# Kernel tuning notes

Hardware: AMD Instinct MI355X
Metric: run time of the kernel (lower is better)

Reference implementation:

```python
import jax, jax.numpy as jnp
import numpy as np

N = 500_000   # total nodes in batched graph
E = 10_000_000  # total edges
G = 1_000     # number of graphs in the batch
H = 8         # hidden_dim
C = 8         # n_classes


def setup_inputs() -> dict:
    key = jax.random.key(0)
    k1, k2, k3, k4, k5, k6 = jax.random.split(key, 6)
    src = jax.random.randint(k1, (E,), 0, N)
    dst = jax.random.randint(k2, (E,), 0, N)
    graph_ids = jnp.sort(jax.random.randint(k3, (N,), 0, G))
    W1 = jax.random.normal(k4, (1, H), dtype=jnp.float32) * 0.5
    W2 = jax.random.normal(k5, (H, H), dtype=jnp.float32) * 0.3
    Wlast = jax.random.normal(k6, (H, C), dtype=jnp.float32) * 0.3
    return {"W1": W1, "W2": W2, "Wlast": Wlast,
            "src": src, "dst": dst, "graph_ids": graph_ids}


def reference(W1, W2, Wlast, src, dst, graph_ids):
    ones_e = jnp.ones(src.shape[0], dtype=jnp.float32)
    deg_in = jax.ops.segment_sum(ones_e, dst, num_segments=N)   # in-degrees
    deg_out = jax.ops.segment_sum(ones_e, src, num_segments=N)  # out-degrees
    # DGL GraphConv norm='both': clamp degrees to >=1, then pow(-1/2)
    inv_sqrt_out = jnp.maximum(deg_out, 1.0) ** -0.5
    inv_sqrt_in = jnp.maximum(deg_in, 1.0) ** -0.5

    def gconv(h, W):
        # h: [N, d]; gather-scatter message passing, then dense transform
        h = h * inv_sqrt_out[:, None]
        agg = jax.ops.segment_sum(h[src], dst, num_segments=N)
        return (agg * inv_sqrt_in[:, None]) @ W

    h = deg_in[:, None]  # input feature = in_degrees, shape [N, 1]
    h = jax.nn.relu(gconv(h, W1))
    h = jax.nn.relu(gconv(h, W2))

    # dgl.mean_nodes: per-graph mean over nodes
    counts = jax.ops.segment_sum(jnp.ones(N, dtype=jnp.float32), graph_ids,
                                 num_segments=G)
    hg = jax.ops.segment_sum(h, graph_ids, num_segments=G)
    hg = hg / jnp.maximum(counts, 1.0)[:, None]
    return hg @ Wlast  # [G, n_classes], Linear with bias=False
```

## Files before the change

kernel.cpp:

```cpp
#include <hip/hip_runtime.h>


#define TB 256
#define DTB 512
#define STB 512
#define BSH 13
#define BNODES 8192
#define MAXNB 64
#define SCH 4096
#define SCH4 (SCH / 4)
#define SCH2 4096
#define EPT 8
#define CSTR 16
#define GLG 4
#define GNUM 16
#define INVB 0xFFFFFFFFu

typedef __attribute__((ext_vector_type(4))) int int4v;
typedef __attribute__((ext_vector_type(4))) unsigned uint4v;
typedef __attribute__((ext_vector_type(2))) unsigned uint2v;
typedef __attribute__((ext_vector_type(4))) float float4v;

__global__ void init_kernel(unsigned* __restrict__ curD, unsigned* __restrict__ curS,
                            unsigned* __restrict__ curC, float* __restrict__ Xsum,
                            int NB, unsigned CAP, int cells, unsigned CAP2, int G) {
    int i = blockIdx.x * TB + threadIdx.x;
    if (i < NB) curD[i * CSTR] = (unsigned)i * CAP;
    if (curS && i < NB) curS[i * CSTR] = (unsigned)i * CAP;
    if (curC && i < cells) curC[i * CSTR] = (unsigned)i * CAP2;
    if (i < G) Xsum[i] = 0.0f;
}

__global__ void scatter_sort_kernel(const int* __restrict__ src, const int* __restrict__ dst,
                                    unsigned* __restrict__ curD, unsigned* __restrict__ curS,
                                    unsigned* __restrict__ dstP, unsigned short* __restrict__ srcP,
                                    int NB, int E, int blk0) {
    __shared__ unsigned cntD[MAXNB], cntS[MAXNB];
    __shared__ unsigned deltaD[MAXNB], deltaS[MAXNB];
    __shared__ unsigned totD_s, totS_s;
    __shared__ unsigned payD[SCH];
    __shared__ unsigned short valS[SCH];
    __shared__ unsigned char mapD[SCH], mapS[SCH];

    int tid = threadIdx.x;
    if (tid < MAXNB) { cntD[tid] = 0u; cntS[tid] = 0u; }
    __syncthreads();

    unsigned sA[EPT], dA[EPT], bD[EPT], bS[EPT];
    int blk = blockIdx.x + blk0;
#pragma unroll
    for (int v = 0; v < 2; ++v) {
        int q = blk * SCH4 + v * STB + tid;
        int be = q * 4;
        if (be + 3 < E) {
            int4v s4 = __builtin_nontemporal_load((const int4v*)src + q);
            int4v d4 = __builtin_nontemporal_load((const int4v*)dst + q);
#pragma unroll
            for (int k = 0; k < 4; ++k) {
                sA[v*4+k] = (unsigned)s4[k];
                dA[v*4+k] = (unsigned)d4[k];
                bD[v*4+k] = dA[v*4+k] >> BSH;
                bS[v*4+k] = sA[v*4+k] >> BSH;
            }
        } else {
#pragma unroll
            for (int k = 0; k < 4; ++k) {
                int j = be + k;
                if (j < E) {
                    sA[v*4+k] = (unsigned)src[j];
                    dA[v*4+k] = (unsigned)dst[j];
                    bD[v*4+k] = dA[v*4+k] >> BSH;
                    bS[v*4+k] = sA[v*4+k] >> BSH;
                } else {
                    bD[v*4+k] = INVB; bS[v*4+k] = INVB;
                    sA[v*4+k] = 0u; dA[v*4+k] = 0u;
                }
            }
        }
    }

#pragma unroll
    for (int k = 0; k < EPT; ++k) {
        if (bD[k] != INVB) {
            atomicAdd(&cntD[bD[k]], 1u);
            if (srcP) atomicAdd(&cntS[bS[k]], 1u);
        }
    }
    __syncthreads();

    int wv = tid >> 6, ln = tid & 63;
    if (wv == 0) {
        unsigned x = (ln < NB) ? cntD[ln] : 0u;
        unsigned inc = x;
#pragma unroll
        for (int o = 1; o < 64; o <<= 1) {
            unsigned y = __shfl_up(inc, o, 64);
            if (ln >= o) inc += y;
        }
        unsigned exc = inc - x;
        if (ln < NB) {
            unsigned gb = atomicAdd(&curD[ln * CSTR], x);
            deltaD[ln] = gb - exc;
            cntD[ln] = exc;
        }
        if (ln == 63) totD_s = inc;
    } else if (wv == 1 && srcP) {
        unsigned x = (ln < NB) ? cntS[ln] : 0u;
        unsigned inc = x;
#pragma unroll
        for (int o = 1; o < 64; o <<= 1) {
            unsigned y = __shfl_up(inc, o, 64);
            if (ln >= o) inc += y;
        }
        unsigned exc = inc - x;
        if (ln < NB) {
            unsigned gb = atomicAdd(&curS[ln * CSTR], x);
            deltaS[ln] = gb - exc;
            cntS[ln] = exc;
        }
        if (ln == 63) totS_s = inc;
    }
    __syncthreads();

#pragma unroll
    for (int k = 0; k < EPT; ++k) {
        if (bD[k] != INVB) {
            unsigned p = atomicAdd(&cntD[bD[k]], 1u);
            payD[p] = ((dA[k] & (BNODES - 1)) << 19) | sA[k];
            mapD[p] = (unsigned char)bD[k];
            if (srcP) {
                unsigned p2 = atomicAdd(&cntS[bS[k]], 1u);
                valS[p2] = (unsigned short)(sA[k] & (BNODES - 1));
                mapS[p2] = (unsigned char)bS[k];
            }
        }
    }
    __syncthreads();

    unsigned tD = totD_s;
    for (unsigned i = tid; i < tD; i += STB) {
        unsigned b = mapD[i];
        dstP[deltaD[b] + i] = payD[i];
    }
    if (srcP) {
        unsigned tS = totS_s;
        for (unsigned i = tid; i < tS; i += STB) {
            unsigned b = mapS[i];
            srcP[deltaS[b] + i] = valS[i];
        }
    }
}

__global__ void subsort_kernel(const unsigned* __restrict__ dstP, const unsigned* __restrict__ curD,
                               unsigned* __restrict__ curC, unsigned* __restrict__ dstP2,
                               unsigned CAP, unsigned CAP2, int NB, int MAXCH) {
    __shared__ unsigned cnt2[MAXNB], delta2[MAXNB];
    __shared__ unsigned tot_s;
    __shared__ unsigned pay[SCH2];
    __shared__ unsigned char map2[SCH2];

    int db = blockIdx.x / MAXCH, c = blockIdx.x % MAXCH;
    unsigned s = (unsigned)db * CAP + (unsigned)c * SCH2;
    unsigned e = curD[db * CSTR];
    if (s >= e) return;
    unsigned n = e - s; if (n > SCH2) n = SCH2;

    int tid = threadIdx.x;
    if (tid < MAXNB) cnt2[tid] = 0u;
    __syncthreads();

    unsigned pl[EPT], bk[EPT];
#pragma unroll
    for (int v = 0; v < 2; ++v) {
        unsigned q = (unsigned)(v * STB + tid);
        unsigned base = q * 4u;
        if (base + 3u < n) {
            uint4v p4 = *((const uint4v*)(dstP + s) + q);
#pragma unroll
            for (int k = 0; k < 4; ++k) {
                pl[v*4+k] = p4[k];
                bk[v*4+k] = (p4[k] & 0x7FFFFu) >> BSH;
            }
        } else {
#pragma unroll
            for (int k = 0; k < 4; ++k) {
                unsigned j = base + (unsigned)k;
                if (j < n) {
                    pl[v*4+k] = dstP[s + j];
                    bk[v*4+k] = (pl[v*4+k] & 0x7FFFFu) >> BSH;
                } else { bk[v*4+k] = INVB; pl[v*4+k] = 0u; }
            }
        }
    }

#pragma unroll
    for (int k = 0; k < EPT; ++k)
        if (bk[k] != INVB) atomicAdd(&cnt2[bk[k]], 1u);
    __syncthreads();

    if (tid < 64) {
        int ln = tid;
        unsigned x = cnt2[ln];
        unsigned inc = x;
#pragma unroll
        for (int o = 1; o < 64; o <<= 1) {
            unsigned y = __shfl_up(inc, o, 64);
            if (ln >= o) inc += y;
        }
        unsigned exc = inc - x;
        if (ln < NB) {
            unsigned gb = atomicAdd(&curC[((unsigned)db * NB + ln) * CSTR], x);
            delta2[ln] = gb - exc;
            cnt2[ln] = exc;
        }
        if (ln == 63) tot_s = inc;
    }
    __syncthreads();

#pragma unroll
    for (int k = 0; k < EPT; ++k) {
        if (bk[k] != INVB) {
            unsigned p = atomicAdd(&cnt2[bk[k]], 1u);
            pay[p] = ((pl[k] >> 19) << BSH) | (pl[k] & (BNODES - 1));
            map2[p] = (unsigned char)bk[k];
        }
    }
    __syncthreads();

    unsigned tot = tot_s;
    for (unsigned i = tid; i < tot; i += STB) {
        unsigned b = map2[i];
        dstP2[delta2[b] + i] = pay[i];
    }
}

__global__ void deg2_kernel(const unsigned* __restrict__ dstP2, const unsigned* __restrict__ curC,
                            unsigned CAP2, unsigned* __restrict__ pDeg, int NB, int GS) {
    __shared__ unsigned h[BNODES];
    {
        uint4v* hv = (uint4v*)h;
        for (int t = threadIdx.x; t < BNODES / 4; t += DTB) hv[t] = (uint4v)0u;
    }
    __syncthreads();
    int b = blockIdx.x >> GLG, g = blockIdx.x & (GNUM - 1);
    int cEnd = (g + 1) * GS; if (cEnd > NB) cEnd = NB;
    for (int c = g * GS; c < cEnd; ++c) {
        unsigned cell = (unsigned)(b * NB + c);
        unsigned lo = cell * CAP2;
        unsigned hi = curC[cell * CSTR];
        unsigned i1 = hi & ~3u;
        const uint4v* qp = (const uint4v*)(dstP2 + lo);
        for (unsigned q = threadIdx.x; q < (i1 - lo) / 4u; q += DTB) {
            uint4v e4 = qp[q];
            atomicAdd(&h[e4.x >> BSH], 0x10000u);
            atomicAdd(&h[e4.y >> BSH], 0x10000u);
            atomicAdd(&h[e4.z >> BSH], 0x10000u);
            atomicAdd(&h[e4.w >> BSH], 0x10000u);
        }
        if (threadIdx.x < hi - i1)
            atomicAdd(&h[dstP2[i1 + threadIdx.x] >> BSH], 0x10000u);
    }
    for (int c = g * GS; c < cEnd; ++c) {
        unsigned cell = (unsigned)(c * NB + b);
        unsigned lo = cell * CAP2;
        unsigned hi = curC[cell * CSTR];
        unsigned i1 = hi & ~3u;
        const uint4v* qp = (const uint4v*)(dstP2 + lo);
        for (unsigned q = threadIdx.x; q < (i1 - lo) / 4u; q += DTB) {
            uint4v e4 = qp[q];
            atomicAdd(&h[e4.x & (BNODES - 1)], 1u);
            atomicAdd(&h[e4.y & (BNODES - 1)], 1u);
            atomicAdd(&h[e4.z & (BNODES - 1)], 1u);
            atomicAdd(&h[e4.w & (BNODES - 1)], 1u);
        }
        if (threadIdx.x < hi - i1)
            atomicAdd(&h[dstP2[i1 + threadIdx.x] & (BNODES - 1)], 1u);
    }
    __syncthreads();
    uint4v* rowv = (uint4v*)(pDeg + (size_t)blockIdx.x * BNODES);
    uint4v* hv = (uint4v*)h;
    for (int t = threadIdx.x; t < BNODES / 4; t += DTB) rowv[t] = hv[t];
}

__global__ void prep2_kernel(const unsigned* __restrict__ pDeg,
                             float* __restrict__ pio, float* __restrict__ h0s,
                             float* __restrict__ isiA, int Npad) {
    int i = blockIdx.x * TB + threadIdx.x;
    if (i >= Npad) return;
    int b = i >> BSH, l = i & (BNODES - 1);
    unsigned din_u = 0, dout_u = 0;
    for (int g = 0; g < GNUM; ++g) {
        unsigned v = __builtin_nontemporal_load(&pDeg[(size_t)(b * GNUM + g) * BNODES + l]);
        din_u  += v >> 16;
        dout_u += v & 0xFFFFu;
    }
    float din = (float)din_u, dout = (float)dout_u;
    float a  = 1.0f / sqrtf(fmaxf(din, 1.0f));
    float bo = 1.0f / sqrtf(fmaxf(dout, 1.0f));
    pio[i]  = a * bo;
    h0s[i]  = din * bo;
    isiA[i] = a;
}

template <int LAST>
__global__ void wh2g_kernel(const unsigned* __restrict__ dstP2, const unsigned* __restrict__ curC,
                            unsigned CAP2, const float* __restrict__ table,
                            float* __restrict__ pOut, int NB, int GS) {
    __shared__ float h[BNODES];
    {
        float4v* hv = (float4v*)h;
        for (int t = threadIdx.x; t < BNODES / 4; t += DTB) hv[t] = (float4v)0.0f;
    }
    __syncthreads();
    int db = blockIdx.x >> GLG, g = blockIdx.x & (GNUM - 1);
    int sbEnd = (g + 1) * GS; if (sbEnd > NB) sbEnd = NB;
    for (int sb = g * GS; sb < sbEnd; ++sb) {
        const float* tb = table + ((size_t)sb << BSH);
        unsigned cell = (unsigned)(db * NB + sb);
        unsigned lo = cell * CAP2;
        unsigned hi = curC[cell * CSTR];
        unsigned i1 = hi & ~3u;
        const uint4v* qp = (const uint4v*)(dstP2 + lo);
        for (unsigned q = threadIdx.x; q < (i1 - lo) / 4u; q += DTB) {
            uint4v e4 = LAST ? __builtin_nontemporal_load(qp + q) : qp[q];
            float t0 = tb[e4.x & (BNODES - 1)];
            float t1 = tb[e4.y & (BNODES - 1)];
            float t2 = tb[e4.z & (BNODES - 1)];
            float t3 = tb[e4.w & (BNODES - 1)];
            atomicAdd(&h[e4.x >> BSH], t0);
            atomicAdd(&h[e4.y >> BSH], t1);
            atomicAdd(&h[e4.z >> BSH], t2);
            atomicAdd(&h[e4.w >> BSH], t3);
        }
        if (threadIdx.x < hi - i1) {
            unsigned e = dstP2[i1 + threadIdx.x];
            atomicAdd(&h[e >> BSH], tb[e & (BNODES - 1)]);
        }
    }
    __syncthreads();
    float4v* rowv = (float4v*)(pOut + (size_t)blockIdx.x * BNODES);
    float4v* hv = (float4v*)h;
    for (int t = threadIdx.x; t < BNODES / 4; t += DTB) rowv[t] = hv[t];
}


__global__ void deghist_kernel(const unsigned short* __restrict__ srcP, const unsigned* __restrict__ dstP,
                               const unsigned* __restrict__ curS, const unsigned* __restrict__ curD,
                               unsigned CAP, unsigned* __restrict__ pDeg, int Jlg) {
    __shared__ unsigned h[BNODES];
    {
        uint4v* hv = (uint4v*)h;
        for (int t = threadIdx.x; t < BNODES / 4; t += DTB) hv[t] = (uint4v)0u;
    }
    __syncthreads();
    int b = blockIdx.x >> Jlg;
    int j = blockIdx.x & ((1 << Jlg) - 1);
    unsigned s0 = (unsigned)b * CAP;
    {
        unsigned cD = curD[b * CSTR] - s0;
        unsigned lo = (unsigned)(((unsigned long long)cD * (unsigned)j) >> Jlg);
        unsigned hi = (unsigned)(((unsigned long long)cD * (unsigned)(j + 1)) >> Jlg);
        for (unsigned i = lo + threadIdx.x; i < hi; i += DTB)
            atomicAdd(&h[dstP[s0 + i] >> 19], 0x10000u);
    }
    {
        unsigned cS = curS[b * CSTR] - s0;
        unsigned lo = (unsigned)(((unsigned long long)cS * (unsigned)j) >> Jlg);
        unsigned hi = (unsigned)(((unsigned long long)cS * (unsigned)(j + 1)) >> Jlg);
        for (unsigned i = lo + threadIdx.x; i < hi; i += DTB)
            atomicAdd(&h[__builtin_nontemporal_load(&srcP[s0 + i])], 1u);
    }
    __syncthreads();
    uint4v* rowv = (uint4v*)(pDeg + (size_t)blockIdx.x * BNODES);
    uint4v* hv = (uint4v*)h;
    for (int t = threadIdx.x; t < BNODES / 4; t += DTB) rowv[t] = hv[t];
}

__global__ void prep_kernel(const unsigned* __restrict__ pDeg,
                            float* __restrict__ pio, float* __restrict__ h0s,
                            float* __restrict__ isiA, int Jlg, int Npad) {
    int i = blockIdx.x * TB + threadIdx.x;
    if (i >= Npad) return;
    int b = i >> BSH, l = i & (BNODES - 1);
    int J = 1 << Jlg;
    unsigned din_u = 0, dout_u = 0;
    for (int j = 0; j < J; ++j) {
        unsigned v = __builtin_nontemporal_load(&pDeg[(size_t)((b << Jlg) + j) * BNODES + l]);
        din_u += v >> 16; dout_u += v & 0xFFFFu;
    }
    float din = (float)din_u, dout = (float)dout_u;
    float a  = 1.0f / sqrtf(fmaxf(din, 1.0f));
    float bo = 1.0f / sqrtf(fmaxf(dout, 1.0f));
    pio[i]  = a * bo;
    h0s[i]  = din * bo;
    isiA[i] = a;
}

template <int LAST>
__global__ void wh_kernel(const unsigned* __restrict__ dstP, const unsigned* __restrict__ curD,
                          unsigned CAP, const float* __restrict__ table,
                          float* __restrict__ pOut, int Jlg) {
    __shared__ float h[BNODES];
    {
        float4v* hv = (float4v*)h;
        for (int t = threadIdx.x; t < BNODES / 4; t += DTB) hv[t] = (float4v)0.0f;
    }
    __syncthreads();
    int b = blockIdx.x >> Jlg;
    int j = blockIdx.x & ((1 << Jlg) - 1);
    unsigned s0 = (unsigned)b * CAP;
    unsigned cD = curD[b * CSTR] - s0;
    unsigned lo = (unsigned)(((unsigned long long)cD * (unsigned)j) >> Jlg);
    unsigned hi = (unsigned)(((unsigned long long)cD * (unsigned)(j + 1)) >> Jlg);
    unsigned i0 = (lo + 3u) & ~3u;
    unsigned i1 = hi & ~3u;
    if (i0 >= i1) {
        for (unsigned i = lo + threadIdx.x; i < hi; i += DTB) {
            unsigned e = dstP[s0 + i];
            atomicAdd(&h[e >> 19], table[e & 0x7FFFFu]);
        }
    } else {
        if (threadIdx.x < i0 - lo) {
            unsigned e = dstP[s0 + lo + threadIdx.x];
            atomicAdd(&h[e >> 19], table[e & 0x7FFFFu]);
        }
        const uint4v* qp = (const uint4v*)(dstP + s0);
        for (unsigned q = i0 / 4u + threadIdx.x; q < i1 / 4u; q += DTB) {
            uint4v e4 = LAST ? __builtin_nontemporal_load(qp + q) : qp[q];
            float t0 = table[e4.x & 0x7FFFFu];
            float t1 = table[e4.y & 0x7FFFFu];
            float t2 = table[e4.z & 0x7FFFFu];
            float t3 = table[e4.w & 0x7FFFFu];
            atomicAdd(&h[e4.x >> 19], t0);
            atomicAdd(&h[e4.y >> 19], t1);
            atomicAdd(&h[e4.z >> 19], t2);
            atomicAdd(&h[e4.w >> 19], t3);
        }
        if (threadIdx.x < hi - i1) {
            unsigned e = dstP[s0 + i1 + threadIdx.x];
            atomicAdd(&h[e >> 19], table[e & 0x7FFFFu]);
        }
    }
    __syncthreads();
    float4v* rowv = (float4v*)(pOut + (size_t)blockIdx.x * BNODES);
    float4v* hv = (float4v*)h;
    for (int t = threadIdx.x; t < BNODES / 4; t += DTB) rowv[t] = hv[t];
}


__global__ void mid_kernel(const float* __restrict__ pC, const float* __restrict__ pio,
                           float* __restrict__ sarr, int Jlg, int Npad) {
    int i = blockIdx.x * TB + threadIdx.x;
    if (i >= Npad) return;
    int b = i >> BSH, l = i & (BNODES - 1);
    int J = 1 << Jlg;
    float t1 = 0.0f;
    for (int j = 0; j < J; ++j)
        t1 += __builtin_nontemporal_load(&pC[(size_t)((b << Jlg) + j) * BNODES + l]);
    sarr[i] = t1 * pio[i];
}

__global__ void poolfinal_kernel(const float* __restrict__ pT, const float* __restrict__ isiA,
                                 const int* __restrict__ graph_ids,
                                 float* __restrict__ Xsum, int Jlg, int N) {
    int i = blockIdx.x * TB + threadIdx.x;
    bool valid = i < N;
    int ii = valid ? i : (N - 1);
    int b = ii >> BSH, l = ii & (BNODES - 1);
    int J = 1 << Jlg;
    float t2 = 0.0f;
    for (int j = 0; j < J; ++j)
        t2 += __builtin_nontemporal_load(&pT[(size_t)((b << Jlg) + j) * BNODES + l]);
    float x = valid ? t2 * isiA[ii] : 0.0f;
    int g = graph_ids[ii];
    int g0 = __shfl(g, 0, 64);
    bool uniform = __all((!valid) || (g == g0));
    if (uniform) {
#pragma unroll
        for (int off = 32; off >= 1; off >>= 1) x += __shfl_down(x, off, 64);
        if ((threadIdx.x & 63) == 0) atomicAdd(&Xsum[g0], x);
    } else if (valid) {
        atomicAdd(&Xsum[g], x);
    }
}

__global__ void final_kernel(const float* __restrict__ Xsum, const int* __restrict__ graph_ids,
                             const float* __restrict__ W1, const float* __restrict__ W2,
                             const float* __restrict__ Wlast,
                             float* __restrict__ out, int N, int GC) {
    int i = blockIdx.x * TB + threadIdx.x;
    if (i < GC) {
        int g = i >> 3, j = i & 7;
        int lo = 0, hi = N;
        while (lo < hi) { int m = (lo + hi) >> 1; if (graph_ids[m] < g) lo = m + 1; else hi = m; }
        int lo2 = lo, hi2 = N;
        while (lo2 < hi2) { int m = (lo2 + hi2) >> 1; if (graph_ids[m] < g + 1) lo2 = m + 1; else hi2 = m; }
        float c = (float)(lo2 - lo);
        float r = 0.0f;
#pragma unroll
        for (int cc = 0; cc < 8; ++cc) {
            float m = 0.0f;
#pragma unroll
            for (int k = 0; k < 8; ++k) m += fmaxf(W1[k], 0.0f) * W2[k * 8 + cc];
            r += fmaxf(m, 0.0f) * Wlast[cc * 8 + j];
        }
        out[i] = Xsum[g] / fmaxf(c, 1.0f) * r;
    }
}


__global__ void fb_deg_kernel(const int* __restrict__ src, const int* __restrict__ dst,
                              float* __restrict__ deg_out, float* __restrict__ deg_in, int E) {
    int i = blockIdx.x * TB + threadIdx.x;
    if (i < E) {
        atomicAdd(&deg_out[src[i]], 1.0f);
        atomicAdd(&deg_in[dst[i]], 1.0f);
    }
}

__global__ void fb_prep_kernel(const float* __restrict__ deg_in, const float* __restrict__ deg_out,
                               float* __restrict__ isi, float* __restrict__ iso,
                               float* __restrict__ h0s, int N) {
    int i = blockIdx.x * TB + threadIdx.x;
    if (i < N) {
        float di = deg_in[i], dn = deg_out[i];
        float a = 1.0f / sqrtf(fmaxf(di, 1.0f));
        float b = 1.0f / sqrtf(fmaxf(dn, 1.0f));
        isi[i] = a; iso[i] = b; h0s[i] = di * b;
    }
}

__global__ void fb_conv_kernel(const int* __restrict__ src, const int* __restrict__ dst,
                               const float* __restrict__ vals, float* __restrict__ t, int E) {
    int i = blockIdx.x * TB + threadIdx.x;
    if (i < E) atomicAdd(&t[dst[i]], vals[src[i]]);
}

__global__ void fb_mid_kernel(const float* __restrict__ agg1, const float* __restrict__ isi,
                              const float* __restrict__ iso, float* __restrict__ s, int N) {
    int i = blockIdx.x * TB + threadIdx.x;
    if (i < N) s[i] = agg1[i] * isi[i] * iso[i];
}

__global__ void fb_pool_kernel(const float* __restrict__ t2, const float* __restrict__ isi,
                               const int* __restrict__ graph_ids,
                               float* __restrict__ Xsum, float* __restrict__ counts, int N) {
    int i = blockIdx.x * TB + threadIdx.x;
    bool valid = i < N;
    int ii = valid ? i : (N - 1);
    float x = valid ? t2[ii] * isi[ii] : 0.0f;
    float cnt = valid ? 1.0f : 0.0f;
    int g = graph_ids[ii];
    int g0 = __shfl(g, 0, 64);
    bool uniform = __all((!valid) || (g == g0));
    if (uniform) {
#pragma unroll
        for (int off = 32; off >= 1; off >>= 1) {
            x += __shfl_down(x, off, 64);
            cnt += __shfl_down(cnt, off, 64);
        }
        if ((threadIdx.x & 63) == 0) { atomicAdd(&Xsum[g0], x); atomicAdd(&counts[g0], cnt); }
    } else if (valid) {
        atomicAdd(&Xsum[g], x); atomicAdd(&counts[g], 1.0f);
    }
}

__global__ void fb_final_kernel(const float* __restrict__ Xsum, const float* __restrict__ counts,
                                const float* __restrict__ W1, const float* __restrict__ W2,
                                const float* __restrict__ Wlast, float* __restrict__ out, int GC) {
    int i = blockIdx.x * TB + threadIdx.x;
    if (i < GC) {
        int g = i >> 3, j = i & 7;
        float r = 0.0f;
#pragma unroll
        for (int c = 0; c < 8; ++c) {
            float m = 0.0f;
#pragma unroll
            for (int k = 0; k < 8; ++k) m += fmaxf(W1[k], 0.0f) * W2[k * 8 + c];
            r += fmaxf(m, 0.0f) * Wlast[c * 8 + j];
        }
        out[i] = Xsum[g] / fmaxf(counts[g], 1.0f) * r;
    }
}


extern "C" void kernel_launch(void* const* d_in, const int* in_sizes, int n_in,
                              void* d_out, int out_size, void* d_ws, size_t ws_size,
                              hipStream_t stream) {
    const float* W1        = (const float*)d_in[0];
    const float* W2        = (const float*)d_in[1];
    const float* Wlast     = (const float*)d_in[2];
    const int*   src       = (const int*)d_in[3];
    const int*   dst       = (const int*)d_in[4];
    const int*   graph_ids = (const int*)d_in[5];
    float* out = (float*)d_out;

    const int E = in_sizes[3];
    const int N = in_sizes[5];
    const int G = out_size / 8;

    int NB   = (N + BNODES - 1) >> BSH;
    int Npad = NB << BSH;
    int NCH  = (E + SCH - 1) / SCH;
    unsigned CAP = (unsigned)(((E / (NB > 0 ? NB : 1)) + 8192 + 511) & ~511);
    char* bp = (char*)d_ws;

    bool fast2D = false;
    size_t q_dstP = 0, q_dstP2 = 0, q_curD = 0, q_curC = 0, q_pio = 0, q_h0sar = 0,
           q_isi = 0, q_Xsum = 0;
    int cells = NB * NB;
    unsigned CAP2 = 0;
    int GS = (NB + GNUM - 1) / GNUM;
    if (N <= (1 << 19) && NB <= MAXNB && E >= 1) {
        CAP2 = (unsigned)(((E / (cells > 0 ? cells : 1)) + 768 + 127) & ~127);
        size_t off = 0;
        auto A = [&](size_t bytes) { size_t o = off; off = (off + bytes + 127) & ~(size_t)127; return o; };
        size_t partBytes = (size_t)NB * GNUM * BNODES * 4;
        size_t dstPBytes = (size_t)NB * CAP * 4;
        q_dstP  = A(dstPBytes > partBytes ? dstPBytes : partBytes);
        q_dstP2 = A((size_t)cells * CAP2 * 4 + (size_t)CAP2 * 4);
        q_curD  = A((size_t)NB * CSTR * 4);
        q_curC  = A((size_t)cells * CSTR * 4);
        q_pio   = A((size_t)Npad * 4);
        q_h0sar = A((size_t)Npad * 4);
        q_isi   = A((size_t)Npad * 4);
        q_Xsum  = A((size_t)G * 4);
        fast2D = (off <= ws_size);
    }

    if (fast2D) {
        unsigned* dstP  = (unsigned*)(bp + q_dstP);
        unsigned* dstP2 = (unsigned*)(bp + q_dstP2);
        unsigned* curD  = (unsigned*)(bp + q_curD);
        unsigned* curC  = (unsigned*)(bp + q_curC);
        unsigned* pDeg  = (unsigned*)(bp + q_dstP);
        float* pC   = (float*)(bp + q_dstP);
        float* pT   = (float*)(bp + q_dstP);
        float* pio  = (float*)(bp + q_pio);
        float* h0s  = (float*)(bp + q_h0sar);
        float* sarr = (float*)(bp + q_h0sar);
        float* isiA = (float*)(bp + q_isi);
        float* Xsum = (float*)(bp + q_Xsum);

        int gridNp = (Npad + TB - 1) / TB;
        int gridN  = (N + TB - 1) / TB;
        int mx = cells > G ? cells : G; if (NB > mx) mx = NB;
        int gridI  = (mx + TB - 1) / TB;
        int MAXCH  = (int)((CAP + SCH2 - 1) / SCH2);
        int NCH1 = (NCH + 1) / 2;
        int NCH2 = NCH - NCH1;

        init_kernel<<<gridI, TB, 0, stream>>>(curD, nullptr, curC, Xsum, NB, CAP, cells, CAP2, G);
        scatter_sort_kernel<<<NCH1, STB, 0, stream>>>(src, dst, curD, nullptr, dstP, nullptr, NB, E, 0);
        if (NCH2 > 0)
            scatter_sort_kernel<<<NCH2, STB, 0, stream>>>(src, dst, curD, nullptr, dstP, nullptr, NB, E, NCH1);
        subsort_kernel<<<NB * MAXCH, STB, 0, stream>>>(dstP, curD, curC, dstP2, CAP, CAP2, NB, MAXCH);
        deg2_kernel<<<NB * GNUM, DTB, 0, stream>>>(dstP2, curC, CAP2, pDeg, NB, GS);
        prep2_kernel<<<gridNp, TB, 0, stream>>>(pDeg, pio, h0s, isiA, Npad);
        wh2g_kernel<0><<<NB * GNUM, DTB, 0, stream>>>(dstP2, curC, CAP2, h0s, pC, NB, GS);
        mid_kernel<<<gridNp, TB, 0, stream>>>(pC, pio, sarr, GLG, Npad);
        wh2g_kernel<1><<<NB * GNUM, DTB, 0, stream>>>(dstP2, curC, CAP2, sarr, pT, NB, GS);
        poolfinal_kernel<<<gridN, TB, 0, stream>>>(pT, isiA, graph_ids, Xsum, GLG, N);
        final_kernel<<<(out_size + TB - 1) / TB, TB, 0, stream>>>(Xsum, graph_ids,
                                                                  W1, W2, Wlast, out, N, out_size);
        return;
    }

    int Jlg = 4;
    size_t req = 0;
    size_t o_dstP, o_srcP, o_curD, o_curS, o_part, o_pio, o_h0sar, o_isi, o_Xsum;
    for (;; --Jlg) {
        int J = 1 << Jlg;
        size_t off = 0;
        auto A = [&](size_t bytes) { size_t o = off; off = (off + bytes + 127) & ~(size_t)127; return o; };
        o_dstP  = A((size_t)NB * CAP * 4);
        o_srcP  = A((size_t)NB * CAP * 2);
        o_curD  = A((size_t)NB * CSTR * 4);
        o_curS  = A((size_t)NB * CSTR * 4);
        o_part  = A((size_t)NB * J * BNODES * 4);
        o_pio   = A((size_t)Npad * 4);
        o_h0sar = A((size_t)Npad * 4);
        o_isi   = A((size_t)Npad * 4);
        o_Xsum  = A((size_t)G * 4);
        req = off;
        if (req <= ws_size || Jlg == 0) break;
    }

    bool fast = (N <= (1 << 19)) && (NB <= MAXNB) && (ws_size >= req) && (E >= 1);

    if (fast) {
        unsigned*       dstP = (unsigned*)(bp + o_dstP);
        unsigned short* srcP = (unsigned short*)(bp + o_srcP);
        unsigned* curD = (unsigned*)(bp + o_curD);
        unsigned* curS = (unsigned*)(bp + o_curS);
        unsigned* pDeg = (unsigned*)(bp + o_part);
        float*    pC   = (float*)(bp + o_part);
        float*    pT   = (float*)(bp + o_part);
        float* pio  = (float*)(bp + o_pio);
        float* h0s  = (float*)(bp + o_h0sar);
        float* sarr = (float*)(bp + o_h0sar);
        float* isiA = (float*)(bp + o_isi);
        float* Xsum = (float*)(bp + o_Xsum);

        int gridNp = (Npad + TB - 1) / TB;
        int gridN  = (N + TB - 1) / TB;
        int J = 1 << Jlg;
        int gridI = ((NB > G ? NB : G) + TB - 1) / TB;
        int NCH1 = (NCH + 1) / 2;
        int NCH2 = NCH - NCH1;

        init_kernel<<<gridI, TB, 0, stream>>>(curD, curS, nullptr, Xsum, NB, CAP, 0, 0, G);
        scatter_sort_kernel<<<NCH1, STB, 0, stream>>>(src, dst, curD, curS, dstP, srcP, NB, E, 0);
        if (NCH2 > 0)
            scatter_sort_kernel<<<NCH2, STB, 0, stream>>>(src, dst, curD, curS, dstP, srcP, NB, E, NCH1);
        deghist_kernel<<<NB * J, DTB, 0, stream>>>(srcP, dstP, curS, curD, CAP, pDeg, Jlg);
        prep_kernel<<<gridNp, TB, 0, stream>>>(pDeg, pio, h0s, isiA, Jlg, Npad);
        wh_kernel<0><<<NB * J, DTB, 0, stream>>>(dstP, curD, CAP, h0s, pC, Jlg);
        mid_kernel<<<gridNp, TB, 0, stream>>>(pC, pio, sarr, Jlg, Npad);
        wh_kernel<1><<<NB * J, DTB, 0, stream>>>(dstP, curD, CAP, sarr, pT, Jlg);
        poolfinal_kernel<<<gridN, TB, 0, stream>>>(pT, isiA, graph_ids, Xsum, Jlg, N);
        final_kernel<<<(out_size + TB - 1) / TB, TB, 0, stream>>>(Xsum, graph_ids,
                                                                  W1, W2, Wlast, out, N, out_size);
    } else {
        float* ws = (float*)d_ws;
        size_t f = 0;
        auto FA = [&](size_t n) { size_t o = f; f += (n + 3) & ~(size_t)3; return o; };
        size_t f_degin  = FA(N);
        size_t f_degout = FA(N);
        size_t f_agg1   = FA(N);
        size_t f_t2     = FA(N);
        size_t f_Xsum   = FA(G);
        size_t f_cnt    = FA(G);
        size_t zf = f;
        size_t f_isi = FA(N);
        size_t f_iso = FA(N);
        size_t f_h0s = FA(N);
        size_t f_s   = FA(N);
        hipMemsetAsync(ws, 0, zf * sizeof(float), stream);
        int gridE = (E + TB - 1) / TB;
        int gridN = (N + TB - 1) / TB;
        int gridO = (out_size + TB - 1) / TB;
        fb_deg_kernel<<<gridE, TB, 0, stream>>>(src, dst, ws + f_degout, ws + f_degin, E);
        fb_prep_kernel<<<gridN, TB, 0, stream>>>(ws + f_degin, ws + f_degout,
                                                 ws + f_isi, ws + f_iso, ws + f_h0s, N);
        fb_conv_kernel<<<gridE, TB, 0, stream>>>(src, dst, ws + f_h0s, ws + f_agg1, E);
        fb_mid_kernel<<<gridN, TB, 0, stream>>>(ws + f_agg1, ws + f_isi, ws + f_iso, ws + f_s, N);
        fb_conv_kernel<<<gridE, TB, 0, stream>>>(src, dst, ws + f_s, ws + f_t2, E);
        fb_pool_kernel<<<gridN, TB, 0, stream>>>(ws + f_t2, ws + f_isi, graph_ids,
                                                 ws + f_Xsum, ws + f_cnt, N);
        fb_final_kernel<<<gridO, TB, 0, stream>>>(ws + f_Xsum, ws + f_cnt, W1, W2, Wlast,
                                                  out, out_size);
    }
}
```

Measured before the change: 391.7 us.

## Split source buckets into 4096-node slices staged in LDS for gathers

The secondary sort now buckets sources into 4096-node slices (up to 128 sub-buckets), so each gather kernel copies the source feature slice into shared memory and reads it from LDS instead of global memory. The degree histogram is split into separate in-degree and out-degree kernels with 16-bit partial outputs, and the group count changes from 16 to 12. The aim is to cut global gather traffic and partial-buffer size. In exchange there are more cells, a two-wave prefix scan, extra syncthreads per slice and one more kernel launch.

```diff
diff --git a/kernel.cpp b/kernel.cpp
--- a/kernel.cpp
+++ b/kernel.cpp
@@ -6,19 +6,21 @@
 #define STB 512
 #define BSH 13
 #define BNODES 8192
+#define BSH2 12
+#define SNODES 4096
 #define MAXNB 64
+#define MAXSB 128
 #define SCH 4096
 #define SCH4 (SCH / 4)
 #define SCH2 4096
 #define EPT 8
 #define CSTR 16
-#define GLG 4
-#define GNUM 16
+#define GNUM 12
+#define GOUT 6
 #define INVB 0xFFFFFFFFu
 
 typedef __attribute__((ext_vector_type(4))) int int4v;
 typedef __attribute__((ext_vector_type(4))) unsigned uint4v;
-typedef __attribute__((ext_vector_type(2))) unsigned uint2v;
 typedef __attribute__((ext_vector_type(4))) float float4v;
 
 __global__ void init_kernel(unsigned* __restrict__ curD, unsigned* __restrict__ curS,
@@ -153,8 +155,9 @@
 
 __global__ void subsort_kernel(const unsigned* __restrict__ dstP, const unsigned* __restrict__ curD,
                                unsigned* __restrict__ curC, unsigned* __restrict__ dstP2,
-                               unsigned CAP, unsigned CAP2, int NB, int MAXCH) {
-    __shared__ unsigned cnt2[MAXNB], delta2[MAXNB];
+                               unsigned CAP, unsigned CAP2, int NSB, int MAXCH) {
+    __shared__ unsigned cnt2[MAXSB], delta2[MAXSB];
+    __shared__ unsigned wtot[2];
     __shared__ unsigned tot_s;
     __shared__ unsigned pay[SCH2];
     __shared__ unsigned char map2[SCH2];
@@ -166,7 +169,7 @@
     unsigned n = e - s; if (n > SCH2) n = SCH2;
 
     int tid = threadIdx.x;
-    if (tid < MAXNB) cnt2[tid] = 0u;
+    if (tid < MAXSB) cnt2[tid] = 0u;
     __syncthreads();
 
     unsigned pl[EPT], bk[EPT];
@@ -179,7 +182,7 @@
 #pragma unroll
             for (int k = 0; k < 4; ++k) {
                 pl[v*4+k] = p4[k];
-                bk[v*4+k] = (p4[k] & 0x7FFFFu) >> BSH;
+                bk[v*4+k] = (p4[k] & 0x7FFFFu) >> BSH2;
             }
         } else {
 #pragma unroll
@@ -187,7 +190,7 @@
                 unsigned j = base + (unsigned)k;
                 if (j < n) {
                     pl[v*4+k] = dstP[s + j];
-                    bk[v*4+k] = (pl[v*4+k] & 0x7FFFFu) >> BSH;
+                    bk[v*4+k] = (pl[v*4+k] & 0x7FFFFu) >> BSH2;
                 } else { bk[v*4+k] = INVB; pl[v*4+k] = 0u; }
             }
         }
@@ -198,22 +201,27 @@
         if (bk[k] != INVB) atomicAdd(&cnt2[bk[k]], 1u);
     __syncthreads();
 
-    if (tid < 64) {
-        int ln = tid;
-        unsigned x = cnt2[ln];
-        unsigned inc = x;
+    unsigned x = 0, inc = 0;
+    if (tid < MAXSB) {
+        x = cnt2[tid];
+        inc = x;
 #pragma unroll
         for (int o = 1; o < 64; o <<= 1) {
             unsigned y = __shfl_up(inc, o, 64);
-            if (ln >= o) inc += y;
-        }
-        unsigned exc = inc - x;
-        if (ln < NB) {
-            unsigned gb = atomicAdd(&curC[((unsigned)db * NB + ln) * CSTR], x);
-            delta2[ln] = gb - exc;
-            cnt2[ln] = exc;
-        }
-        if (ln == 63) tot_s = inc;
+            if ((tid & 63) >= o) inc += y;
+        }
+        if ((tid & 63) == 63) wtot[tid >> 6] = inc;
+    }
+    __syncthreads();
+    if (tid < MAXSB) {
+        unsigned base = (tid >= 64) ? wtot[0] : 0u;
+        unsigned exc = inc - x + base;
+        if (tid < NSB) {
+            unsigned gb = atomicAdd(&curC[((unsigned)db * NSB + tid) * CSTR], x);
+            delta2[tid] = gb - exc;
+            cnt2[tid] = exc;
+        }
+        if (tid == MAXSB - 1) tot_s = inc + base;
     }
     __syncthreads();
 
@@ -221,7 +229,7 @@
     for (int k = 0; k < EPT; ++k) {
         if (bk[k] != INVB) {
             unsigned p = atomicAdd(&cnt2[bk[k]], 1u);
-            pay[p] = ((pl[k] >> 19) << BSH) | (pl[k] & (BNODES - 1));
+            pay[p] = ((pl[k] >> 19) << BSH2) | (pl[k] & (SNODES - 1));
             map2[p] = (unsigned char)bk[k];
         }
     }
@@ -234,65 +242,83 @@
     }
 }
 
-__global__ void deg2_kernel(const unsigned* __restrict__ dstP2, const unsigned* __restrict__ curC,
-                            unsigned CAP2, unsigned* __restrict__ pDeg, int NB, int GS) {
+__global__ void degin2_kernel(const unsigned* __restrict__ dstP2, const unsigned* __restrict__ curC,
+                              unsigned CAP2, unsigned short* __restrict__ pDegIn, int NSB, int GS) {
     __shared__ unsigned h[BNODES];
     {
         uint4v* hv = (uint4v*)h;
         for (int t = threadIdx.x; t < BNODES / 4; t += DTB) hv[t] = (uint4v)0u;
     }
     __syncthreads();
-    int b = blockIdx.x >> GLG, g = blockIdx.x & (GNUM - 1);
-    int cEnd = (g + 1) * GS; if (cEnd > NB) cEnd = NB;
-    for (int c = g * GS; c < cEnd; ++c) {
-        unsigned cell = (unsigned)(b * NB + c);
+    int db = blockIdx.x / GNUM, g = blockIdx.x % GNUM;
+    int sbEnd = (g + 1) * GS; if (sbEnd > NSB) sbEnd = NSB;
+    for (int sb = g * GS; sb < sbEnd; ++sb) {
+        unsigned cell = (unsigned)(db * NSB + sb);
         unsigned lo = cell * CAP2;
         unsigned hi = curC[cell * CSTR];
         unsigned i1 = hi & ~3u;
         const uint4v* qp = (const uint4v*)(dstP2 + lo);
         for (unsigned q = threadIdx.x; q < (i1 - lo) / 4u; q += DTB) {
             uint4v e4 = qp[q];
-            atomicAdd(&h[e4.x >> BSH], 0x10000u);
-            atomicAdd(&h[e4.y >> BSH], 0x10000u);
-            atomicAdd(&h[e4.z >> BSH], 0x10000u);
-            atomicAdd(&h[e4.w >> BSH], 0x10000u);
+            atomicAdd(&h[e4.x >> BSH2], 1u);
+            atomicAdd(&h[e4.y >> BSH2], 1u);
+            atomicAdd(&h[e4.z >> BSH2], 1u);
+            atomicAdd(&h[e4.w >> BSH2], 1u);
         }
         if (threadIdx.x < hi - i1)
-            atomicAdd(&h[dstP2[i1 + threadIdx.x] >> BSH], 0x10000u);
-    }
-    for (int c = g * GS; c < cEnd; ++c) {
-        unsigned cell = (unsigned)(c * NB + b);
+            atomicAdd(&h[dstP2[i1 + threadIdx.x] >> BSH2], 1u);
+    }
+    __syncthreads();
+    unsigned short* row = pDegIn + (size_t)blockIdx.x * BNODES;
+    for (int t = threadIdx.x; t < BNODES; t += DTB) row[t] = (unsigned short)h[t];
+}
+
+__global__ void degout2_kernel(const unsigned* __restrict__ dstP2, const unsigned* __restrict__ curC,
+                               unsigned CAP2, unsigned short* __restrict__ pDegOut,
+                               int NSB, int NB, int GS) {
+    __shared__ unsigned h[SNODES];
+    {
+        uint4v* hv = (uint4v*)h;
+        for (int t = threadIdx.x; t < SNODES / 4; t += DTB) hv[t] = (uint4v)0u;
+    }
+    __syncthreads();
+    int sb = blockIdx.x / GOUT, g = blockIdx.x % GOUT;
+    int dbEnd = (g + 1) * GS; if (dbEnd > NB) dbEnd = NB;
+    for (int db = g * GS; db < dbEnd; ++db) {
+        unsigned cell = (unsigned)(db * NSB + sb);
         unsigned lo = cell * CAP2;
         unsigned hi = curC[cell * CSTR];
         unsigned i1 = hi & ~3u;
         const uint4v* qp = (const uint4v*)(dstP2 + lo);
         for (unsigned q = threadIdx.x; q < (i1 - lo) / 4u; q += DTB) {
             uint4v e4 = qp[q];
-            atomicAdd(&h[e4.x & (BNODES - 1)], 1u);
-            atomicAdd(&h[e4.y & (BNODES - 1)], 1u);
-            atomicAdd(&h[e4.z & (BNODES - 1)], 1u);
-            atomicAdd(&h[e4.w & (BNODES - 1)], 1u);
+            atomicAdd(&h[e4.x & (SNODES - 1)], 1u);
+            atomicAdd(&h[e4.y & (SNODES - 1)], 1u);
+            atomicAdd(&h[e4.z & (SNODES - 1)], 1u);
+            atomicAdd(&h[e4.w & (SNODES - 1)], 1u);
         }
         if (threadIdx.x < hi - i1)
-            atomicAdd(&h[dstP2[i1 + threadIdx.x] & (BNODES - 1)], 1u);
-    }
-    __syncthreads();
-    uint4v* rowv = (uint4v*)(pDeg + (size_t)blockIdx.x * BNODES);
-    uint4v* hv = (uint4v*)h;
-    for (int t = threadIdx.x; t < BNODES / 4; t += DTB) rowv[t] = hv[t];
-}
-
-__global__ void prep2_kernel(const unsigned* __restrict__ pDeg,
+            atomicAdd(&h[dstP2[i1 + threadIdx.x] & (SNODES - 1)], 1u);
+    }
+    __syncthreads();
+    unsigned short* row = pDegOut + (size_t)blockIdx.x * SNODES;
+    for (int t = threadIdx.x; t < SNODES; t += DTB) row[t] = (unsigned short)h[t];
+}
+
+__global__ void prep2_kernel(const unsigned short* __restrict__ pDegIn,
+                             const unsigned short* __restrict__ pDegOut,
                              float* __restrict__ pio, float* __restrict__ h0s,
-                             float* __restrict__ isiA, int Npad) {
+                             float* __restrict__ isiA, int NSB, int N, int Npad) {
     int i = blockIdx.x * TB + threadIdx.x;
     if (i >= Npad) return;
-    int b = i >> BSH, l = i & (BNODES - 1);
+    int db = i >> BSH, l13 = i & (BNODES - 1);
     unsigned din_u = 0, dout_u = 0;
-    for (int g = 0; g < GNUM; ++g) {
-        unsigned v = __builtin_nontemporal_load(&pDeg[(size_t)(b * GNUM + g) * BNODES + l]);
-        din_u  += v >> 16;
-        dout_u += v & 0xFFFFu;
+    for (int g = 0; g < GNUM; ++g)
+        din_u += pDegIn[(size_t)(db * GNUM + g) * BNODES + l13];
+    if (i < N) {
+        int sb = i >> BSH2, l12 = i & (SNODES - 1);
+        for (int g = 0; g < GOUT; ++g)
+            dout_u += pDegOut[(size_t)(sb * GOUT + g) * SNODES + l12];
     }
     float din = (float)din_u, dout = (float)dout_u;
     float a  = 1.0f / sqrtf(fmaxf(din, 1.0f));
@@ -303,38 +329,44 @@
 }
 
 template <int LAST>
-__global__ void wh2g_kernel(const unsigned* __restrict__ dstP2, const unsigned* __restrict__ curC,
+__global__ void wh2s_kernel(const unsigned* __restrict__ dstP2, const unsigned* __restrict__ curC,
                             unsigned CAP2, const float* __restrict__ table,
-                            float* __restrict__ pOut, int NB, int GS) {
+                            float* __restrict__ pOut, int NSB, int GS) {
     __shared__ float h[BNODES];
+    __shared__ float slice[SNODES];
     {
         float4v* hv = (float4v*)h;
         for (int t = threadIdx.x; t < BNODES / 4; t += DTB) hv[t] = (float4v)0.0f;
     }
-    __syncthreads();
-    int db = blockIdx.x >> GLG, g = blockIdx.x & (GNUM - 1);
-    int sbEnd = (g + 1) * GS; if (sbEnd > NB) sbEnd = NB;
+    int db = blockIdx.x / GNUM, g = blockIdx.x % GNUM;
+    int sbEnd = (g + 1) * GS; if (sbEnd > NSB) sbEnd = NSB;
     for (int sb = g * GS; sb < sbEnd; ++sb) {
-        const float* tb = table + ((size_t)sb << BSH);
-        unsigned cell = (unsigned)(db * NB + sb);
+        __syncthreads();
+        {
+            const float4v* tp = (const float4v*)(table + ((size_t)sb << BSH2));
+            float4v* sp = (float4v*)slice;
+            for (int t = threadIdx.x; t < SNODES / 4; t += DTB) sp[t] = tp[t];
+        }
+        __syncthreads();
+        unsigned cell = (unsigned)(db * NSB + sb);
         unsigned lo = cell * CAP2;
         unsigned hi = curC[cell * CSTR];
         unsigned i1 = hi & ~3u;
         const uint4v* qp = (const uint4v*)(dstP2 + lo);
         for (unsigned q = threadIdx.x; q < (i1 - lo) / 4u; q += DTB) {
             uint4v e4 = LAST ? __builtin_nontemporal_load(qp + q) : qp[q];
-            float t0 = tb[e4.x & (BNODES - 1)];
-            float t1 = tb[e4.y & (BNODES - 1)];
-            float t2 = tb[e4.z & (BNODES - 1)];
-            float t3 = tb[e4.w & (BNODES - 1)];
-            atomicAdd(&h[e4.x >> BSH], t0);
-            atomicAdd(&h[e4.y >> BSH], t1);
-            atomicAdd(&h[e4.z >> BSH], t2);
-            atomicAdd(&h[e4.w >> BSH], t3);
+            float t0 = slice[e4.x & (SNODES - 1)];
+            float t1 = slice[e4.y & (SNODES - 1)];
+            float t2 = slice[e4.z & (SNODES - 1)];
+            float t3 = slice[e4.w & (SNODES - 1)];
+            atomicAdd(&h[e4.x >> BSH2], t0);
+            atomicAdd(&h[e4.y >> BSH2], t1);
+            atomicAdd(&h[e4.z >> BSH2], t2);
+            atomicAdd(&h[e4.w >> BSH2], t3);
         }
         if (threadIdx.x < hi - i1) {
             unsigned e = dstP2[i1 + threadIdx.x];
-            atomicAdd(&h[e >> BSH], tb[e & (BNODES - 1)]);
+            atomicAdd(&h[e >> BSH2], slice[e & (SNODES - 1)]);
         }
     }
     __syncthreads();
@@ -449,28 +481,26 @@
 
 
 __global__ void mid_kernel(const float* __restrict__ pC, const float* __restrict__ pio,
-                           float* __restrict__ sarr, int Jlg, int Npad) {
+                           float* __restrict__ sarr, int J, int Npad) {
     int i = blockIdx.x * TB + threadIdx.x;
     if (i >= Npad) return;
     int b = i >> BSH, l = i & (BNODES - 1);
-    int J = 1 << Jlg;
     float t1 = 0.0f;
     for (int j = 0; j < J; ++j)
-        t1 += __builtin_nontemporal_load(&pC[(size_t)((b << Jlg) + j) * BNODES + l]);
+        t1 += __builtin_nontemporal_load(&pC[(size_t)(b * J + j) * BNODES + l]);
     sarr[i] = t1 * pio[i];
 }
 
 __global__ void poolfinal_kernel(const float* __restrict__ pT, const float* __restrict__ isiA,
                                  const int* __restrict__ graph_ids,
-                                 float* __restrict__ Xsum, int Jlg, int N) {
+                                 float* __restrict__ Xsum, int J, int N) {
     int i = blockIdx.x * TB + threadIdx.x;
     bool valid = i < N;
     int ii = valid ? i : (N - 1);
     int b = ii >> BSH, l = ii & (BNODES - 1);
-    int J = 1 << Jlg;
     float t2 = 0.0f;
     for (int j = 0; j < J; ++j)
-        t2 += __builtin_nontemporal_load(&pT[(size_t)((b << Jlg) + j) * BNODES + l]);
+        t2 += __builtin_nontemporal_load(&pT[(size_t)(b * J + j) * BNODES + l]);
     float x = valid ? t2 * isiA[ii] : 0.0f;
     int g = graph_ids[ii];
     int g0 = __shfl(g, 0, 64);
@@ -606,18 +636,26 @@
     char* bp = (char*)d_ws;
 
     bool fast2D = false;
-    size_t q_dstP = 0, q_dstP2 = 0, q_curD = 0, q_curC = 0, q_pio = 0, q_h0sar = 0,
+    size_t q_reg1 = 0, q_dstP2 = 0, q_curD = 0, q_curC = 0, q_pio = 0, q_h0sar = 0,
            q_isi = 0, q_Xsum = 0;
-    int cells = NB * NB;
+    size_t degInBytes = 0;
+    int NSB = (N + SNODES - 1) >> BSH2;
+    int cells = NB * NSB;
     unsigned CAP2 = 0;
-    int GS = (NB + GNUM - 1) / GNUM;
-    if (N <= (1 << 19) && NB <= MAXNB && E >= 1) {
-        CAP2 = (unsigned)(((E / (cells > 0 ? cells : 1)) + 768 + 127) & ~127);
+    int GS_sb = (NSB + GNUM - 1) / GNUM;
+    int GS_db = (NB + GOUT - 1) / GOUT;
+    if (N <= (1 << 19) && NB <= MAXNB && NSB <= MAXSB && E >= 1) {
+        CAP2 = (unsigned)(((E / (cells > 0 ? cells : 1)) + 384 + 127) & ~127);
+        degInBytes = (size_t)NB * GNUM * BNODES * 2;
+        size_t degOutBytes = (size_t)NSB * GOUT * SNODES * 2;
+        size_t pCBytes = (size_t)NB * GNUM * BNODES * 4;
+        size_t dstPBytes = (size_t)NB * CAP * 4;
+        size_t reg1 = dstPBytes;
+        if (degInBytes + degOutBytes > reg1) reg1 = degInBytes + degOutBytes;
+        if (pCBytes > reg1) reg1 = pCBytes;
         size_t off = 0;
         auto A = [&](size_t bytes) { size_t o = off; off = (off + bytes + 127) & ~(size_t)127; return o; };
-        size_t partBytes = (size_t)NB * GNUM * BNODES * 4;
-        size_t dstPBytes = (size_t)NB * CAP * 4;
-        q_dstP  = A(dstPBytes > partBytes ? dstPBytes : partBytes);
+        q_reg1  = A(reg1);
         q_dstP2 = A((size_t)cells * CAP2 * 4 + (size_t)CAP2 * 4);
         q_curD  = A((size_t)NB * CSTR * 4);
         q_curC  = A((size_t)cells * CSTR * 4);
@@ -629,13 +667,14 @@
     }
 
     if (fast2D) {
-        unsigned* dstP  = (unsigned*)(bp + q_dstP);
+        unsigned* dstP  = (unsigned*)(bp + q_reg1);
         unsigned* dstP2 = (unsigned*)(bp + q_dstP2);
         unsigned* curD  = (unsigned*)(bp + q_curD);
         unsigned* curC  = (unsigned*)(bp + q_curC);
-        unsigned* pDeg  = (unsigned*)(bp + q_dstP);
-        float* pC   = (float*)(bp + q_dstP);
-        float* pT   = (float*)(bp + q_dstP);
+        unsigned short* pDegIn  = (unsigned short*)(bp + q_reg1);
+        unsigned short* pDegOut = (unsigned short*)(bp + q_reg1 + degInBytes);
+        float* pC   = (float*)(bp + q_reg1);
+        float* pT   = (float*)(bp + q_reg1);
         float* pio  = (float*)(bp + q_pio);
         float* h0s  = (float*)(bp + q_h0sar);
         float* sarr = (float*)(bp + q_h0sar);
@@ -654,13 +693,14 @@
         scatter_sort_kernel<<<NCH1, STB, 0, stream>>>(src, dst, curD, nullptr, dstP, nullptr, NB, E, 0);
         if (NCH2 > 0)
             scatter_sort_kernel<<<NCH2, STB, 0, stream>>>(src, dst, curD, nullptr, dstP, nullptr, NB, E, NCH1);
-        subsort_kernel<<<NB * MAXCH, STB, 0, stream>>>(dstP, curD, curC, dstP2, CAP, CAP2, NB, MAXCH);
-        deg2_kernel<<<NB * GNUM, DTB, 0, stream>>>(dstP2, curC, CAP2, pDeg, NB, GS);
-        prep2_kernel<<<gridNp, TB, 0, stream>>>(pDeg, pio, h0s, isiA, Npad);
-        wh2g_kernel<0><<<NB * GNUM, DTB, 0, stream>>>(dstP2, curC, CAP2, h0s, pC, NB, GS);
-        mid_kernel<<<gridNp, TB, 0, stream>>>(pC, pio, sarr, GLG, Npad);
-        wh2g_kernel<1><<<NB * GNUM, DTB, 0, stream>>>(dstP2, curC, CAP2, sarr, pT, NB, GS);
-        poolfinal_kernel<<<gridN, TB, 0, stream>>>(pT, isiA, graph_ids, Xsum, GLG, N);
+        subsort_kernel<<<NB * MAXCH, STB, 0, stream>>>(dstP, curD, curC, dstP2, CAP, CAP2, NSB, MAXCH);
+        degin2_kernel<<<NB * GNUM, DTB, 0, stream>>>(dstP2, curC, CAP2, pDegIn, NSB, GS_sb);
+        degout2_kernel<<<NSB * GOUT, DTB, 0, stream>>>(dstP2, curC, CAP2, pDegOut, NSB, NB, GS_db);
+        prep2_kernel<<<gridNp, TB, 0, stream>>>(pDegIn, pDegOut, pio, h0s, isiA, NSB, N, Npad);
+        wh2s_kernel<0><<<NB * GNUM, DTB, 0, stream>>>(dstP2, curC, CAP2, h0s, pC, NSB, GS_sb);
+        mid_kernel<<<gridNp, TB, 0, stream>>>(pC, pio, sarr, GNUM, Npad);
+        wh2s_kernel<1><<<NB * GNUM, DTB, 0, stream>>>(dstP2, curC, CAP2, sarr, pT, NSB, GS_sb);
+        poolfinal_kernel<<<gridN, TB, 0, stream>>>(pT, isiA, graph_ids, Xsum, GNUM, N);
         final_kernel<<<(out_size + TB - 1) / TB, TB, 0, stream>>>(Xsum, graph_ids,
                                                                   W1, W2, Wlast, out, N, out_size);
         return;
@@ -716,9 +756,9 @@
         deghist_kernel<<<NB * J, DTB, 0, stream>>>(srcP, dstP, curS, curD, CAP, pDeg, Jlg);
         prep_kernel<<<gridNp, TB, 0, stream>>>(pDeg, pio, h0s, isiA, Jlg, Npad);
         wh_kernel<0><<<NB * J, DTB, 0, stream>>>(dstP, curD, CAP, h0s, pC, Jlg);
-        mid_kernel<<<gridNp, TB, 0, stream>>>(pC, pio, sarr, Jlg, Npad);
+        mid_kernel<<<gridNp, TB, 0, stream>>>(pC, pio, sarr, J, Npad);
         wh_kernel<1><<<NB * J, DTB, 0, stream>>>(dstP, curD, CAP, sarr, pT, Jlg);
-        poolfinal_kernel<<<gridN, TB, 0, stream>>>(pT, isiA, graph_ids, Xsum, Jlg, N);
+        poolfinal_kernel<<<gridN, TB, 0, stream>>>(pT, isiA, graph_ids, Xsum, J, N);
         final_kernel<<<(out_size + TB - 1) / TB, TB, 0, stream>>>(Xsum, graph_ids,
                                                                   W1, W2, Wlast, out, N, out_size);
     } else {
```

Measured after the change: 423.8 us. +8.2%, slower.
